# Kernel optimization log

Hardware: AMD Instinct MI355X
Metric: run time of the kernel (lower is better)

## Reference

```python
import jax, jax.numpy as jnp
import numpy as np

T, N, C, RADIUS = 64, 16, 256, 64
D_OUT = 2 * RADIUS + 1
TAU = 2.0
DECAY = float(np.exp(-1.0 / TAU))  # first-order leaky (LIF) filter decay
WEIGHT0 = 6.53543197272069


def setup_inputs() -> dict:
    key = jax.random.key(0)
    k1, k2 = jax.random.split(key)
    inp = jax.random.uniform(k1, (T, N, C, 2), dtype=jnp.float32)
    delay_param = jnp.arange(-RADIUS, RADIUS + 1, dtype=jnp.float32)[:, None]  # (D_out, 1)
    weight = jnp.asarray(WEIGHT0, dtype=jnp.float32)
    u = jax.random.uniform(k2, (N, C, D_OUT, 2), dtype=jnp.float32)  # bernoulli uniforms
    return {"input": inp, "delay_param": delay_param, "weight": weight, "u": u}


def reference(input, delay_param, weight, u):
    Tn, Nn, Cn, _ = input.shape
    # delay = relu(cat([_delay, -_delay], dim=1))  -> (D_out, 2), nonnegative
    delay = jax.nn.relu(jnp.concatenate([delay_param, -delay_param], axis=1))
    Do = delay.shape[0]
    # input.unsqueeze(-2).repeat(..., D_out, 1) -> (T, N, C, D_out, 2)
    x = jnp.broadcast_to(input[:, :, :, None, :], (Tn, Nn, Cn, Do, 2))
    # stochastic rounding of per-synapse delay
    bd = jnp.broadcast_to(delay[None, None], (Nn, Cn, Do, 2))
    df = jnp.floor(bd)
    rounded = jnp.where(u < bd - df, df + 1.0, df)
    # clamp so the (one-hot) spike at argmax(t) stays inside the window
    spike_t = jnp.argmax(x, axis=0)  # (N, C, D_out, 2)
    rounded = jnp.minimum(rounded, (Tn - 1 - spike_t).astype(rounded.dtype))
    d = rounded.astype(jnp.int32)
    # circular shift along time: out[t] = x[(t - d) % T]
    t_idx = jnp.arange(Tn)[:, None, None, None, None]
    idx = (t_idx - d[None]) % Tn
    shifted = jnp.take_along_axis(x, idx, axis=0)  # (T, N, C, D_out, 2)
    # LIF filter (leaky integrator over time, state reset at t=0)
    def step(v, xt):
        v = v * DECAY + xt
        return v, v
    _, filt = jax.lax.scan(step, jnp.zeros_like(shifted[0]), shifted)
    # scale by fixed synaptic weight and sum over the 2 input channels
    return jnp.sum(filt * weight, axis=-1)  # (T, N, C, D_out)
```

## Files before the change

kernel.cpp:

```cpp
#include <hip/hip_runtime.h>

#define T_DIM 64
#define NP 4096
#define D_OUTC 129
#define ROW_STRIDE (NP * D_OUTC)
#define PPB 4

typedef float v2f __attribute__((ext_vector_type(2)));

__global__ __launch_bounds__(256, 4) void jeffress_kernel(
    const float* __restrict__ input,
    const float* __restrict__ delay_param,
    const float* __restrict__ weight,
    const float* __restrict__ u,
    float* __restrict__ out)
{
    __shared__ float Hw[PPB * 2 * 128];
    __shared__ int caps[PPB][2];

    const int blk = blockIdx.x;
    const int g   = ((blk & 7) << 7) | (blk >> 3);
    const int p0  = g * PPB;
    const int tid = threadIdx.x;
    const int lane = tid & 63, wv = tid >> 6;
    const float DECAY = 0.6065306597126334f;
    const float w = weight[0];

    {
        float2 xp = ((const float2*)input)[lane * NP + p0 + wv];
        #pragma unroll
        for (int ch = 0; ch < 2; ++ch) {
            float xv = ch ? xp.y : xp.x;
            unsigned b = __float_as_uint(xv);
            b ^= (b & 0x80000000u) ? 0xffffffffu : 0x80000000u;
            unsigned long long key = ((unsigned long long)b << 32) | (unsigned)(63 - lane);
            #pragma unroll
            for (int mm = 1; mm < 64; mm <<= 1) {
                unsigned long long o = __shfl_xor(key, mm, 64);
                if (o > key) key = o;
            }
            if (lane == 0) caps[wv][ch] = (int)(key & 0xffffffffull);
        }
        float v0 = xp.x, v1 = xp.y;
        const float dks[6] = {0.6065306597126334f,
                              0.36787944117144233f,
                              0.1353352832366127f,
                              0.01831563888873418f,
                              3.3546262790251185e-4f,
                              1.1253517471925912e-7f};
        #pragma unroll
        for (int k = 0; k < 6; ++k) {
            int o = 1 << k;
            float q0 = __shfl_up(v0, o, 64);
            float q1 = __shfl_up(v1, o, 64);
            if (lane >= o) { v0 += dks[k] * q0; v1 += dks[k] * q1; }
        }
        float h063 = __shfl(v0, 63, 64);
        float h163 = __shfl(v1, 63, 64);
        float f = exp2f(-0.7213475204444817f * (float)(lane + 1));
        float* H0 = &Hw[(wv * 2 + 0) * 128];
        float* H1 = &Hw[(wv * 2 + 1) * 128];
        H0[lane] = w * v0;  H0[64 + lane] = w * (v0 + f * h063);
        H1[lane] = w * v1;  H1[64 + lane] = w * (v1 + f * h163);
    }
    __syncthreads();

    auto mke = [&](int q, int& o0, int& o1, float& Cw) {
        int pl = q / 129;
        int d  = q - 129 * pl;
        float dp = delay_param[d];
        float b0 = fmaxf(dp, 0.0f), b1 = fmaxf(-dp, 0.0f);
        float2 uu = ((const float2*)u)[(p0 + pl) * D_OUTC + d];
        float f0 = floorf(b0), f1 = floorf(b1);
        float r0 = (uu.x < b0 - f0) ? f0 + 1.0f : f0;
        float r1 = (uu.y < b1 - f1) ? f1 + 1.0f : f1;
        int s0 = (int)fminf(r0, (float)caps[pl][0]);
        int s1 = (int)fminf(r1, (float)caps[pl][1]);
        o0 = (pl * 2 + 0) * 128 + 64 - s0;
        o1 = (pl * 2 + 1) * 128 + 64 - s1;
        Cw = Hw[o0 - 1] + Hw[o1 - 1];
    };

    int oA0, oA1, oB0, oB1; float CwA, CwB;
    mke(2 * tid,     oA0, oA1, CwA);
    mke(2 * tid + 1, oB0, oB1, CwB);
    const bool xtra = (tid < 2);
    int oC0 = 0, oC1 = 0, oD0 = 0, oD1 = 0; float CwC = 0.0f, CwDd = 0.0f;
    if (xtra) {
        mke(512 + 2 * tid, oC0, oC1, CwC);
        mke(513 + 2 * tid, oD0, oD1, CwDd);
    }

    float* rp  = out + (size_t)p0 * D_OUTC + 2 * tid;
    float* rpx = out + (size_t)p0 * D_OUTC + 512 + 2 * tid;

    const float K[8] = {1.0f, 0.6065306597126334f, 0.36787944117144233f,
                        0.22313016014842982f, 0.1353352832366127f,
                        0.0820849986238988f, 0.049787068367863944f,
                        0.030197383422318501f};
    float Dg = DECAY;

    for (int tg = 0; tg < T_DIM; tg += 8) {
        float cA = CwA * Dg, cB = CwB * Dg;
        float cC = CwC * Dg, cD = CwDd * Dg;
        #pragma unroll
        for (int j = 0; j < 8; ++j) {
            int t = tg + j;
            v2f v;
            v.x = Hw[oA0 + t] + Hw[oA1 + t] - K[j] * cA;
            v.y = Hw[oB0 + t] + Hw[oB1 + t] - K[j] * cB;
            *(v2f*)(rp + (size_t)t * ROW_STRIDE) = v;
            if (xtra) {
                v2f vx;
                vx.x = Hw[oC0 + t] + Hw[oC1 + t] - K[j] * cC;
                vx.y = Hw[oD0 + t] + Hw[oD1 + t] - K[j] * cD;
                *(v2f*)(rpx + (size_t)t * ROW_STRIDE) = vx;
            }
        }
        Dg *= 0.01831563888873418f;
    }
}

extern "C" void kernel_launch(void* const* d_in, const int* in_sizes, int n_in,
                              void* d_out, int out_size, void* d_ws, size_t ws_size,
                              hipStream_t stream) {
    const float* input       = (const float*)d_in[0];
    const float* delay_param = (const float*)d_in[1];
    const float* weight      = (const float*)d_in[2];
    const float* u           = (const float*)d_in[3];
    float* out = (float*)d_out;

    jeffress_kernel<<<NP / PPB, 256, 0, stream>>>(input, delay_param, weight, u, out);
}
```

Measured before the change: 156.4 us.

## Split time axis across two blocks, dedupe LDS reads, use nontemporal stores

Launches twice as many blocks, each handling half of the 64 timesteps, and recomputes the shared prefix-filter setup in each. Reorders the per-delay offsets so the channel whose delay is zero is shared between adjacent outputs, which skips a redundant LDS read when they match. Switches output writes to nontemporal stores and raises the occupancy hint. The cost is duplicated setup work (argmax shuffles, scans, LDS fill) per block.

```diff
diff --git a/kernel.cpp b/kernel.cpp
--- a/kernel.cpp
+++ b/kernel.cpp
@@ -5,10 +5,12 @@
 #define D_OUTC 129
 #define ROW_STRIDE (NP * D_OUTC)
 #define PPB 4
+#define NBLK_P (NP / PPB)
+#define TSPLIT 2
 
 typedef float v2f __attribute__((ext_vector_type(2)));
 
-__global__ __launch_bounds__(256, 4) void jeffress_kernel(
+__global__ __launch_bounds__(256, 6) void jeffress_kernel(
     const float* __restrict__ input,
     const float* __restrict__ delay_param,
     const float* __restrict__ weight,
@@ -19,7 +21,9 @@
     __shared__ int caps[PPB][2];
 
     const int blk = blockIdx.x;
-    const int g   = ((blk & 7) << 7) | (blk >> 3);
+    const int gb  = blk & (NBLK_P - 1);
+    const int th  = blk >> 10;
+    const int g   = ((gb & 7) << 7) | (gb >> 3);
     const int p0  = g * PPB;
     const int tid = threadIdx.x;
     const int lane = tid & 63, wv = tid >> 6;
@@ -65,7 +69,7 @@
     }
     __syncthreads();
 
-    auto mke = [&](int q, int& o0, int& o1, float& Cw) {
+    auto mke = [&](int q, int& ov, int& ou, float& Cw) {
         int pl = q / 129;
         int d  = q - 129 * pl;
         float dp = delay_param[d];
@@ -76,19 +80,23 @@
         float r1 = (uu.y < b1 - f1) ? f1 + 1.0f : f1;
         int s0 = (int)fminf(r0, (float)caps[pl][0]);
         int s1 = (int)fminf(r1, (float)caps[pl][1]);
-        o0 = (pl * 2 + 0) * 128 + 64 - s0;
-        o1 = (pl * 2 + 1) * 128 + 64 - s1;
-        Cw = Hw[o0 - 1] + Hw[o1 - 1];
+        int o0 = (pl * 2 + 0) * 128 + 64 - s0;
+        int o1 = (pl * 2 + 1) * 128 + 64 - s1;
+        if (d <= 64) { ou = o0; ov = o1; } else { ou = o1; ov = o0; }
+        Cw = Hw[ov - 1] + Hw[ou - 1];
     };
 
-    int oA0, oA1, oB0, oB1; float CwA, CwB;
-    mke(2 * tid,     oA0, oA1, CwA);
-    mke(2 * tid + 1, oB0, oB1, CwB);
+    int oAv, oAu, oBv, oBu; float CwA, CwB;
+    mke(2 * tid,     oAv, oAu, CwA);
+    mke(2 * tid + 1, oBv, oBu, CwB);
+    const bool sameAB = (oAu == oBu);
     const bool xtra = (tid < 2);
-    int oC0 = 0, oC1 = 0, oD0 = 0, oD1 = 0; float CwC = 0.0f, CwDd = 0.0f;
+    int oCv = 0, oCu = 0, oDv = 0, oDu = 0; float CwC = 0.0f, CwDd = 0.0f;
+    bool sameCD = true;
     if (xtra) {
-        mke(512 + 2 * tid, oC0, oC1, CwC);
-        mke(513 + 2 * tid, oD0, oD1, CwDd);
+        mke(512 + 2 * tid, oCv, oCu, CwC);
+        mke(513 + 2 * tid, oDv, oDu, CwDd);
+        sameCD = (oCu == oDu);
     }
 
     float* rp  = out + (size_t)p0 * D_OUTC + 2 * tid;
@@ -98,23 +106,30 @@
                         0.22313016014842982f, 0.1353352832366127f,
                         0.0820849986238988f, 0.049787068367863944f,
                         0.030197383422318501f};
-    float Dg = DECAY;
+    float Dg = th ? DECAY * 1.1253517471925912e-7f : DECAY;
 
-    for (int tg = 0; tg < T_DIM; tg += 8) {
+    const int t0 = th << 5;
+    for (int tg = t0; tg < t0 + 32; tg += 8) {
         float cA = CwA * Dg, cB = CwB * Dg;
         float cC = CwC * Dg, cD = CwDd * Dg;
         #pragma unroll
         for (int j = 0; j < 8; ++j) {
             int t = tg + j;
+            float uA = Hw[oAu + t];
+            float uB = uA;
+            if (!sameAB) uB = Hw[oBu + t];
             v2f v;
-            v.x = Hw[oA0 + t] + Hw[oA1 + t] - K[j] * cA;
-            v.y = Hw[oB0 + t] + Hw[oB1 + t] - K[j] * cB;
-            *(v2f*)(rp + (size_t)t * ROW_STRIDE) = v;
+            v.x = Hw[oAv + t] + uA - K[j] * cA;
+            v.y = Hw[oBv + t] + uB - K[j] * cB;
+            __builtin_nontemporal_store(v, (v2f*)(rp + (size_t)t * ROW_STRIDE));
             if (xtra) {
+                float uC = Hw[oCu + t];
+                float uD = uC;
+                if (!sameCD) uD = Hw[oDu + t];
                 v2f vx;
-                vx.x = Hw[oC0 + t] + Hw[oC1 + t] - K[j] * cC;
-                vx.y = Hw[oD0 + t] + Hw[oD1 + t] - K[j] * cD;
-                *(v2f*)(rpx + (size_t)t * ROW_STRIDE) = vx;
+                vx.x = Hw[oCv + t] + uC - K[j] * cC;
+                vx.y = Hw[oDv + t] + uD - K[j] * cD;
+                __builtin_nontemporal_store(vx, (v2f*)(rpx + (size_t)t * ROW_STRIDE));
             }
         }
         Dg *= 0.01831563888873418f;
@@ -130,5 +145,5 @@
     const float* u           = (const float*)d_in[3];
     float* out = (float*)d_out;
 
-    jeffress_kernel<<<NP / PPB, 256, 0, stream>>>(input, delay_param, weight, u, out);
+    jeffress_kernel<<<NBLK_P * TSPLIT, 256, 0, stream>>>(input, delay_param, weight, u, out);
 }
```

After: 177.4 us. 1.13x slower.
